# Kernel tuning notes

Measured on AMD Instinct MI355X. Metric: run time of the kernel, lower is better.

Reference implementation:

```python
import jax, jax.numpy as jnp
import numpy as np

N, E, G, Hd, Fin, L, C = 50000, 600000, 1024, 128, 74, 5, 2


def _gru(x, h, w_ih, w_hh, b_ih, b_hh):
    gi = x @ w_ih.T + b_ih
    gh = h @ w_hh.T + b_hh
    ir, iz, inn = jnp.split(gi, 3, axis=-1)
    hr, hz, hn = jnp.split(gh, 3, axis=-1)
    r = jax.nn.sigmoid(ir + hr)
    z = jax.nn.sigmoid(iz + hz)
    n = jnp.tanh(inn + r * hn)
    return (1.0 - z) * n + z * h


def _lstm_scan(xs, w_ih, w_hh, b_ih, b_hh):
    # xs: [T, B, Din]; PyTorch gate order i, f, g, o
    B = xs.shape[1]
    H = w_hh.shape[1]
    def step(carry, x):
        h, c = carry
        g = x @ w_ih.T + h @ w_hh.T + (b_ih + b_hh)
        i, f, gg, o = jnp.split(g, 4, axis=-1)
        c = jax.nn.sigmoid(f) * c + jax.nn.sigmoid(i) * jnp.tanh(gg)
        h = jax.nn.sigmoid(o) * jnp.tanh(c)
        return (h, c), h
    init = (jnp.zeros((B, H), xs.dtype), jnp.zeros((B, H), xs.dtype))
    _, ys = jax.lax.scan(step, init, xs)
    return ys


def setup_inputs():
    key = jax.random.key(0)
    ks = jax.random.split(key, 32)
    s = 0.05
    d = {}
    d['feats'] = jax.random.normal(ks[0], (N, Fin), jnp.float32)
    d['src'] = jax.random.randint(ks[1], (E,), 0, N)
    d['dst'] = jax.random.randint(ks[2], (E,), 0, N)
    d['node2graph'] = jnp.sort(jax.random.randint(ks[3], (N,), 0, G))
    d['W_in'] = jax.random.normal(ks[4], (Fin, Hd), jnp.float32) * s
    d['b_in'] = jnp.zeros((Hd,), jnp.float32)
    d['bn_gamma'] = jnp.ones((L, Hd), jnp.float32)
    d['bn_beta'] = jnp.zeros((L, Hd), jnp.float32)
    d['bn_mean'] = jax.random.normal(ks[5], (L, Hd), jnp.float32) * 0.1
    d['bn_var'] = jax.random.uniform(ks[6], (L, Hd), jnp.float32, 0.5, 1.5)
    d['gru_w_ih'] = jax.random.normal(ks[7], (3 * Hd, 2 * Hd), jnp.float32) * s
    d['gru_w_hh'] = jax.random.normal(ks[8], (3 * Hd, Hd), jnp.float32) * s
    d['gru_b_ih'] = jnp.zeros((3 * Hd,), jnp.float32)
    d['gru_b_hh'] = jnp.zeros((3 * Hd,), jnp.float32)
    d['w_aw'] = jax.random.normal(ks[9], (Hd, 1), jnp.float32) * s
    d['b_aw'] = jnp.zeros((1,), jnp.float32)
    d['lw_ih_f'] = jax.random.normal(ks[10], (4 * Hd, 2 * Hd), jnp.float32) * s
    d['lw_hh_f'] = jax.random.normal(ks[11], (4 * Hd, Hd), jnp.float32) * s
    d['lb_ih_f'] = jnp.zeros((4 * Hd,), jnp.float32)
    d['lb_hh_f'] = jnp.zeros((4 * Hd,), jnp.float32)
    d['lw_ih_b'] = jax.random.normal(ks[12], (4 * Hd, 2 * Hd), jnp.float32) * s
    d['lw_hh_b'] = jax.random.normal(ks[13], (4 * Hd, Hd), jnp.float32) * s
    d['lb_ih_b'] = jnp.zeros((4 * Hd,), jnp.float32)
    d['lb_hh_b'] = jnp.zeros((4 * Hd,), jnp.float32)
    d['W_out'] = jax.random.normal(ks[14], (2 * Hd, C), jnp.float32) * s
    d['b_out'] = jnp.zeros((C,), jnp.float32)
    return d


def reference(feats, src, dst, node2graph, W_in, b_in, bn_gamma, bn_beta, bn_mean, bn_var,
              gru_w_ih, gru_w_hh, gru_b_ih, gru_b_hh, w_aw, b_aw,
              lw_ih_f, lw_hh_f, lb_ih_f, lb_hh_f, lw_ih_b, lw_hh_b, lb_ih_b, lb_hh_b,
              W_out, b_out):
    gin_eps = 1e-5
    h = feats @ W_in + b_in  # [N, Hd]
    reps = []
    for l in range(L):
        # BatchNorm1d (eval mode, running stats)
        x = (h - bn_mean[l]) * jax.lax.rsqrt(bn_var[l] + 1e-5) * bn_gamma[l] + bn_beta[l]
        # GIN sum aggregation over edges (src -> dst)
        agg = jax.ops.segment_sum(x[src], dst, num_segments=N)  # [N, Hd]
        # GRUCell apply_func: input = concat([(1+eps)*feat, agg]), hidden = feat
        hc = _gru(jnp.concatenate([(1.0 + gin_eps) * x, agg], axis=-1), x,
                  gru_w_ih, gru_w_hh, gru_b_ih, gru_b_hh)
        hc = jax.nn.celu(hc)
        # WeightedSumAndMax readout on pre-BN feats (h)
        w = jax.nn.sigmoid(h @ w_aw + b_aw)  # [N, 1]
        ws = jax.ops.segment_sum(w * h, node2graph, num_segments=G)
        hm = jax.ops.segment_max(h, node2graph, num_segments=G)
        hm = jnp.where(jnp.isfinite(hm), hm, 0.0)
        reps.append(jnp.concatenate([ws, hm], axis=-1))  # [G, 2Hd]
        h = hc + h  # residual
    rep = jnp.stack(reps, axis=0)  # [L, G, 2Hd]
    y_f = _lstm_scan(rep, lw_ih_f, lw_hh_f, lb_ih_f, lb_hh_f)
    y_b = _lstm_scan(rep[::-1], lw_ih_b, lw_hh_b, lb_ih_b, lb_hh_b)[::-1]
    out0 = jnp.concatenate([y_f[0], y_b[0]], axis=-1)  # lstm output at t=0, [G, 2Hd]
    return out0 @ W_out + b_out  # [G, C]
```

## Files before the change

### kernel.cpp

```cpp
#include <hip/hip_runtime.h>
#include <math.h>

#define NN 50000
#define NP 50048
#define NE 600000
#define NG 1024
#define NL 5
#define NT (NP / 64)
#define GRUGRID 256

typedef __attribute__((ext_vector_type(8))) short bfrag8;
typedef __attribute__((ext_vector_type(4))) float f32x4;

__device__ __forceinline__ float fexp_(float x) { return __builtin_amdgcn_exp2f(x * 1.44269504f); }
__device__ __forceinline__ float sig_(float x)  { return __builtin_amdgcn_rcpf(1.f + fexp_(-x)); }
__device__ __forceinline__ float ftanh_(float x){ return fmaf(2.f, __builtin_amdgcn_rcpf(1.f + fexp_(-2.f * x)), -1.f); }
__device__ __forceinline__ float fexpm1_(float x){ return fexp_(x) - 1.f; }

__device__ __forceinline__ unsigned short bf16r_(float x) {
  union { float f; unsigned u; } v; v.f = x;
  unsigned u = v.u;
  return (unsigned short)((u + 0x7FFFu + ((u >> 16) & 1u)) >> 16);
}
__device__ __forceinline__ float bf16tof_(unsigned short h) {
  union { float f; unsigned u; } v; v.u = ((unsigned)h) << 16;
  return v.f;
}

__device__ __forceinline__ void gl_lds16(const unsigned short* g, unsigned short* l) {
  __builtin_amdgcn_global_load_lds(
      (const __attribute__((address_space(1))) unsigned int*)g,
      (__attribute__((address_space(3))) unsigned int*)l, 16, 0, 0);
}

__global__ __launch_bounds__(256) void k_input_proj(
    const float* __restrict__ feats, const float* __restrict__ W_in,
    const float* __restrict__ b_in, float* __restrict__ h)
{
  const int j = threadIdx.x & 127;
  const int half = threadIdx.x >> 7;
  float wcol[74];
#pragma unroll
  for (int k = 0; k < 74; ++k) wcol[k] = W_in[k * 128 + j];
  const float bj = b_in[j];
  for (int p = blockIdx.x; p < NN / 2; p += gridDim.x) {
    int node = __builtin_amdgcn_readfirstlane(p * 2 + half);
    const float* fr = feats + (size_t)node * 74;
    float acc = bj;
#pragma unroll
    for (int k = 0; k < 74; ++k) acc = fmaf(fr[k], wcol[k], acc);
    h[(size_t)node * 128 + j] = acc;
  }
}

__global__ void k_bnprep_all(const float* __restrict__ g, const float* __restrict__ b,
                             const float* __restrict__ m, const float* __restrict__ v,
                             float* __restrict__ bnp)
{
  int l = blockIdx.x;
  int j = threadIdx.x;
  float s = g[l * 128 + j] * rsqrtf(v[l * 128 + j] + 1e-5f);
  bnp[l * 256 + j] = s;
  bnp[l * 256 + 128 + j] = b[l * 128 + j] - m[l * 128 + j] * s;
}

__global__ __launch_bounds__(256) void k_wpack(
    const float* __restrict__ w_ih, const float* __restrict__ w_hh,
    const float* __restrict__ b_ih, const float* __restrict__ b_hh,
    unsigned short* __restrict__ Wp, float* __restrict__ bcat)
{
  int idx = blockIdx.x * 256 + threadIdx.x;
  int n = idx >> 8, k = idx & 255;
  float val;
  if (n < 256) {
    val = (k < 128) ? fmaf(1.00001f, w_ih[n * 256 + k], w_hh[n * 128 + k])
                    : w_ih[n * 256 + k];
  } else if (n < 384) {
    val = (k < 128) ? 1.00001f * w_ih[n * 256 + k] : w_ih[n * 256 + k];
  } else {
    int g = n - 128;
    val = (k < 128) ? w_hh[g * 128 + k] : 0.f;
  }
  Wp[(size_t)(k >> 5) * 16384 + n * 32 + (k & 31)] = bf16r_(val);
  if (k == 0) {
    float bc;
    if (n < 256) bc = b_ih[n] + b_hh[n];
    else if (n < 384) bc = b_ih[n];
    else bc = b_hh[n - 128];
    bcat[n] = bc;
  }
}

__global__ __launch_bounds__(256) void k_wpack_lstm(
    const float* __restrict__ lwih_f, const float* __restrict__ lwih_b,
    const float* __restrict__ lwhh_b,
    const float* __restrict__ lbih_f, const float* __restrict__ lbhh_f,
    const float* __restrict__ lbih_b, const float* __restrict__ lbhh_b,
    unsigned short* __restrict__ Wihf, unsigned short* __restrict__ Wihb,
    unsigned short* __restrict__ Whhb, float* __restrict__ bcf, float* __restrict__ bcb)
{
  int idx = blockIdx.x * 256 + threadIdx.x;
  if (idx < 131072) {
    int n = idx >> 8, k = idx & 255;
    Wihf[(size_t)(k >> 5) * 16384 + n * 32 + (k & 31)] = bf16r_(lwih_f[n * 256 + k]);
  } else if (idx < 262144) {
    int i2 = idx - 131072; int n = i2 >> 8, k = i2 & 255;
    Wihb[(size_t)(k >> 5) * 16384 + n * 32 + (k & 31)] = bf16r_(lwih_b[n * 256 + k]);
  } else if (idx < 327680) {
    int i2 = idx - 262144; int n = i2 >> 7, k = i2 & 127;
    Whhb[(size_t)(k >> 5) * 16384 + n * 32 + (k & 31)] = bf16r_(lwhh_b[n * 128 + k]);
  }
  if (idx < 512) {
    bcf[idx] = lbih_f[idx] + lbhh_f[idx];
    bcb[idx] = lbih_b[idx] + lbhh_b[idx];
  }
}

__global__ __launch_bounds__(256) void k_prep(
    const float* __restrict__ h, const float* __restrict__ bnp,
    const float* __restrict__ w_aw, const float* __restrict__ b_aw,
    unsigned short* __restrict__ xhi, float* __restrict__ wnode)
{
  int t = blockIdx.x * 256 + threadIdx.x;
  int row = t >> 4, c = t & 15;
  const float* hp = h + (size_t)row * 128 + c * 8;
  float4 h0 = *(const float4*)(hp);
  float4 h1 = *(const float4*)(hp + 4);
  float4 s0 = *(const float4*)(bnp + c * 8);
  float4 s1 = *(const float4*)(bnp + c * 8 + 4);
  float4 t0 = *(const float4*)(bnp + 128 + c * 8);
  float4 t1 = *(const float4*)(bnp + 128 + c * 8 + 4);
  float x[8] = { fmaf(h0.x, s0.x, t0.x), fmaf(h0.y, s0.y, t0.y),
                 fmaf(h0.z, s0.z, t0.z), fmaf(h0.w, s0.w, t0.w),
                 fmaf(h1.x, s1.x, t1.x), fmaf(h1.y, s1.y, t1.y),
                 fmaf(h1.z, s1.z, t1.z), fmaf(h1.w, s1.w, t1.w) };
  unsigned hiw[4];
#pragma unroll
  for (int i = 0; i < 4; ++i) {
    unsigned short ha = bf16r_(x[2 * i]), hb = bf16r_(x[2 * i + 1]);
    hiw[i] = (unsigned)ha | ((unsigned)hb << 16);
  }
  size_t dst = (size_t)row * 16 + (c ^ (row & 7));
  ((uint4*)xhi)[dst] = make_uint4(hiw[0], hiw[1], hiw[2], hiw[3]);
  const float4 wa0 = *(const float4*)(w_aw + c * 8);
  const float4 wa1 = *(const float4*)(w_aw + c * 8 + 4);
  float p = h0.x * wa0.x + h0.y * wa0.y + h0.z * wa0.z + h0.w * wa0.w +
            h1.x * wa1.x + h1.y * wa1.y + h1.z * wa1.z + h1.w * wa1.w;
#pragma unroll
  for (int o = 8; o > 0; o >>= 1) p += __shfl_xor(p, o);
  if (c == 0) wnode[row] = sig_(p + b_aw[0]);
}

__global__ __launch_bounds__(256) void k_hist(const int* __restrict__ dst, int* __restrict__ deg)
{
  int t = blockIdx.x * 256 + threadIdx.x;
  if (t < NE) atomicAdd(&deg[dst[t]], 1);
}

__global__ __launch_bounds__(256) void k_scan1(const int* __restrict__ deg, int* __restrict__ bsum)
{
  __shared__ int red[4];
  int i = blockIdx.x * 256 + threadIdx.x;
  int d = (i < NN) ? deg[i] : 0;
  int s = d;
#pragma unroll
  for (int o = 32; o > 0; o >>= 1) s += __shfl_xor(s, o);
  if ((threadIdx.x & 63) == 0) red[threadIdx.x >> 6] = s;
  __syncthreads();
  if (threadIdx.x == 0) bsum[blockIdx.x] = red[0] + red[1] + red[2] + red[3];
}

__global__ __launch_bounds__(256) void k_scan2(const int* __restrict__ bsum, int* __restrict__ boff,
                                               int* __restrict__ rowptr)
{
  __shared__ int part[256];
  int t = threadIdx.x;
  int v = (t < 196) ? bsum[t] : 0;
  part[t] = v;
  __syncthreads();
  for (int o = 1; o < 256; o <<= 1) {
    int u = (t >= o) ? part[t - o] : 0;
    __syncthreads();
    part[t] += u;
    __syncthreads();
  }
  if (t < 196) boff[t] = part[t] - v;
  if (t == 0) rowptr[NN] = NE;
}

__global__ __launch_bounds__(256) void k_scan3(const int* __restrict__ deg, const int* __restrict__ boff,
                                               int* __restrict__ rowptr)
{
  __shared__ int part[256];
  int t = threadIdx.x;
  int i = blockIdx.x * 256 + t;
  int d = (i < NN) ? deg[i] : 0;
  part[t] = d;
  __syncthreads();
  for (int o = 1; o < 256; o <<= 1) {
    int u = (t >= o) ? part[t - o] : 0;
    __syncthreads();
    part[t] += u;
    __syncthreads();
  }
  if (i < NN) rowptr[i] = boff[blockIdx.x] + part[t] - d;
}

__global__ __launch_bounds__(256) void k_fill(
    const int* __restrict__ src, const int* __restrict__ dst,
    int* __restrict__ pos, int* __restrict__ col)
{
  int t = blockIdx.x * 256 + threadIdx.x;
  if (t >= NE) return;
  int p = atomicAdd(&pos[dst[t]], 1);
  col[p] = src[t];
}

__global__ __launch_bounds__(256) void k_gather(
    const unsigned short* __restrict__ xhi, const int* __restrict__ rowptr,
    const int* __restrict__ col, unsigned short* __restrict__ agghi)
{
  int n = blockIdx.x * 4 + (threadIdx.x >> 6);
  int lane = threadIdx.x & 63;
  int c = lane >> 2, q = lane & 3;
  int lo = rowptr[n], hi = rowptr[n + 1];
  const unsigned* xp = (const unsigned*)xhi;
  float a0 = 0.f, a1 = 0.f, a2 = 0.f, a3 = 0.f;
  float b0 = 0.f, b1 = 0.f, b2 = 0.f, b3 = 0.f;
  int e = lo;
  for (; e + 3 < hi; e += 4) {
    int r0 = col[e], r1 = col[e + 1], r2 = col[e + 2], r3 = col[e + 3];
    unsigned u0 = xp[(size_t)r0 * 64 + ((c ^ (r0 & 7)) << 2) + q];
    unsigned u1 = xp[(size_t)r1 * 64 + ((c ^ (r1 & 7)) << 2) + q];
    unsigned u2 = xp[(size_t)r2 * 64 + ((c ^ (r2 & 7)) << 2) + q];
    unsigned u3 = xp[(size_t)r3 * 64 + ((c ^ (r3 & 7)) << 2) + q];
    a0 += bf16tof_((unsigned short)(u0 & 0xFFFF)); b0 += bf16tof_((unsigned short)(u0 >> 16));
    a1 += bf16tof_((unsigned short)(u1 & 0xFFFF)); b1 += bf16tof_((unsigned short)(u1 >> 16));
    a2 += bf16tof_((unsigned short)(u2 & 0xFFFF)); b2 += bf16tof_((unsigned short)(u2 >> 16));
    a3 += bf16tof_((unsigned short)(u3 & 0xFFFF)); b3 += bf16tof_((unsigned short)(u3 >> 16));
  }
  for (; e < hi; ++e) {
    int r0 = col[e];
    unsigned u0 = xp[(size_t)r0 * 64 + ((c ^ (r0 & 7)) << 2) + q];
    a0 += bf16tof_((unsigned short)(u0 & 0xFFFF));
    b0 += bf16tof_((unsigned short)(u0 >> 16));
  }
  float s0 = (a0 + a1) + (a2 + a3), s1 = (b0 + b1) + (b2 + b3);
  unsigned short h0 = bf16r_(s0), h1 = bf16r_(s1);
  size_t w = (size_t)n * 64 + ((c ^ (n & 7)) << 2) + q;
  ((unsigned*)agghi)[w] = (unsigned)h0 | ((unsigned)h1 << 16);
}

__device__ __forceinline__ int lbound_(const int* __restrict__ a, int n, int key)
{
  int lo = 0, hi = n;
  while (lo < hi) { int mid = (lo + hi) >> 1; if (a[mid] < key) lo = mid + 1; else hi = mid; }
  return lo;
}

__global__ __launch_bounds__(256) void k_readout(
    const float* __restrict__ h, const float* __restrict__ wnode,
    const int* __restrict__ n2g, unsigned short* __restrict__ xplh,
    unsigned short* __restrict__ xpll, int layer)
{
  __shared__ float WS[128], HM[128];
  int g = blockIdx.x;
  int tid = threadIdx.x;
  int j = tid & 127, ty = tid >> 7;
  int lo = lbound_(n2g, NN, g);
  int hi = lbound_(n2g, NN, g + 1);
  float ws0 = 0.f, hm0 = -INFINITY, ws1 = 0.f, hm1 = -INFINITY;
  int n = lo + ty;
  for (; n + 2 < hi; n += 4) {
    float hv0 = h[(size_t)n * 128 + j];
    float hv1 = h[(size_t)(n + 2) * 128 + j];
    ws0 = fmaf(wnode[n], hv0, ws0);     hm0 = fmaxf(hm0, hv0);
    ws1 = fmaf(wnode[n + 2], hv1, ws1); hm1 = fmaxf(hm1, hv1);
  }
  if (n < hi) {
    float hv0 = h[(size_t)n * 128 + j];
    ws0 = fmaf(wnode[n], hv0, ws0); hm0 = fmaxf(hm0, hv0);
  }
  float ws = ws0 + ws1, hm = fmaxf(hm0, hm1);
  if (ty == 1) { WS[j] = ws; HM[j] = hm; }
  __syncthreads();
  if (ty == 0) {
    ws += WS[j];
    hm = fmaxf(hm, HM[j]);
    if (hi == lo) hm = 0.f;
    int r = layer * NG + g;
    {
      unsigned short hi16 = bf16r_(ws);
      unsigned short lo16 = bf16r_(ws - bf16tof_(hi16));
      size_t si = (size_t)r * 256 + (((j >> 3) ^ (r & 7)) << 3) + (j & 7);
      xplh[si] = hi16; xpll[si] = lo16;
    }
    {
      int ch = 128 + j;
      unsigned short hi16 = bf16r_(hm);
      unsigned short lo16 = bf16r_(hm - bf16tof_(hi16));
      size_t si = (size_t)r * 256 + (((ch >> 3) ^ (r & 7)) << 3) + (ch & 7);
      xplh[si] = hi16; xpll[si] = lo16;
    }
  }
}

__global__ __launch_bounds__(512, 2) void k_gru_mfma(
    float* __restrict__ h,
    const unsigned short* __restrict__ xhi, const unsigned short* __restrict__ agghi,
    const unsigned short* __restrict__ Wp, const float* __restrict__ bcat,
    const float* __restrict__ bnp)
{
  __shared__ alignas(16) unsigned short A[2][16384];
  const int tid = threadIdx.x;
  const int lane = tid & 63;
  const int wv = tid >> 6;
  const int mfr = lane & 15;
  const int kq = lane >> 4;
  const int j = wv * 16 + mfr;

  bfrag8 wreg[8][4];
#pragma unroll
  for (int kb = 0; kb < 8; ++kb) {
    int ng = (kb < 4) ? 4 : 3;
#pragma unroll
    for (int g = 0; g < 4; ++g) {
      if (g < ng) {
        int n = g * 128 + j;
        wreg[kb][g] = *(const bfrag8*)(Wp + (size_t)kb * 16384 + n * 32 + kq * 8);
      }
    }
  }

  auto stage = [&](int buf, int tile) {
    size_t goff = (size_t)tile * 64 * 128;
    const unsigned short* srcs[2] = { xhi + goff, agghi + goff };
#pragma unroll
    for (int p = 0; p < 2; ++p) {
#pragma unroll
      for (int it = 0; it < 2; ++it) {
        int off = it * 4096 + wv * 512;
        gl_lds16(srcs[p] + off + lane * 8, &A[buf][p * 8192 + off]);
      }
    }
  };

  const float sc = bnp[j], sh = bnp[128 + j];
  const float br = bcat[j], bz = bcat[128 + j], bi = bcat[256 + j], bh = bcat[384 + j];

  int tile = blockIdx.x;
  stage(0, tile);
  __syncthreads();
  int cur = 0;

  while (true) {
    int nxt = tile + GRUGRID;
    int m0 = tile * 64;

    float hvr[4][4];
#pragma unroll
    for (int m = 0; m < 4; ++m)
#pragma unroll
      for (int reg = 0; reg < 4; ++reg)
        hvr[m][reg] = h[(size_t)(m0 + m * 16 + kq * 4 + reg) * 128 + j];

    if (nxt < NT) stage(cur ^ 1, nxt);

    f32x4 acc[4][4];
#pragma unroll
    for (int m = 0; m < 4; ++m)
#pragma unroll
      for (int g = 0; g < 4; ++g) acc[m][g] = (f32x4){0.f, 0.f, 0.f, 0.f};

    const char* Ab = (const char*)&A[cur][0];
#pragma unroll
    for (int kb = 0; kb < 8; ++kb) {
      int kp = kb & 3;
      int hoff = (kb < 4) ? 0 : 16384;
      int ng = (kb < 4) ? 4 : 3;
      bfrag8 ah[4];
#pragma unroll
      for (int m = 0; m < 4; ++m) {
        int row = m * 16 + mfr;
        int cs = (((kp * 4 + kq) ^ (row & 7)) << 4);
        ah[m] = *(const bfrag8*)(Ab + hoff + row * 256 + cs);
      }
#pragma unroll
      for (int m = 0; m < 4; ++m)
#pragma unroll
        for (int g = 0; g < 4; ++g) {
          if (g < ng)
            acc[m][g] = __builtin_amdgcn_mfma_f32_16x16x32_bf16(ah[m], wreg[kb][g], acc[m][g], 0, 0, 0);
        }
    }

    float hnew[4][4];
#pragma unroll
    for (int m = 0; m < 4; ++m) {
#pragma unroll
      for (int reg = 0; reg < 4; ++reg) {
        float hvv = hvr[m][reg];
        float x = fmaf(hvv, sc, sh);
        float r = sig_(acc[m][0][reg] + br);
        float z = sig_(acc[m][1][reg] + bz);
        float n2 = ftanh_(fmaf(r, acc[m][3][reg] + bh, acc[m][2][reg] + bi));
        float o = (1.f - z) * n2 + z * x;
        float hc = (o > 0.f) ? o : fexpm1_(o);
        hnew[m][reg] = hvv + hc;
      }
    }

    __syncthreads();

    float* Hst = (float*)&A[cur][0];
#pragma unroll
    for (int m = 0; m < 4; ++m)
#pragma unroll
      for (int reg = 0; reg < 4; ++reg) {
        int nl = m * 16 + kq * 4 + reg;
        Hst[nl * 128 + (j ^ ((nl & 7) << 2))] = hnew[m][reg];
      }

    __syncthreads();

    {
      float* dst = h + (size_t)m0 * 128;
#pragma unroll
      for (int p = 0; p < 4; ++p) {
        int b = p * 2048 + tid * 4;
        int row = b >> 7;
        int off = b & 127;
        float4 v = *(const float4*)&Hst[row * 128 + (off ^ ((row & 7) << 2))];
        *(float4*)&dst[b] = v;
      }
    }

    if (nxt >= NT) break;
    __syncthreads();
    cur ^= 1;
    tile = nxt;
  }
}

__global__ __launch_bounds__(512) void k_xgates(
    const unsigned short* __restrict__ xplh, const unsigned short* __restrict__ xpll,
    const unsigned short* __restrict__ Wihb, const unsigned short* __restrict__ Wihf,
    const float* __restrict__ bcb, const float* __restrict__ bcf,
    float* __restrict__ gxb, float* __restrict__ gxf)
{
  __shared__ alignas(16) unsigned short Ah[16384], Al[16384];
  int bid = blockIdx.x;
  const unsigned short* Wp; const float* bc; float* gx; int r0;
  if (bid < 80) { Wp = Wihb; bc = bcb; gx = gxb; r0 = bid * 64; }
  else          { Wp = Wihf; bc = bcf; gx = gxf; r0 = (bid - 80) * 64; }
  const int tid = threadIdx.x;
  const int lane = tid & 63;
  const int wv = tid >> 6;
  const int mfr = lane & 15;
  const int kq = lane >> 4;
  const int j = wv * 16 + mfr;

#pragma unroll
  for (int q = 0; q < 4; ++q) {
    int off = (q * 512 + wv * 64) * 8;
    gl_lds16(xplh + (size_t)r0 * 256 + off + lane * 8, &Ah[off]);
    gl_lds16(xpll + (size_t)r0 * 256 + off + lane * 8, &Al[off]);
  }

  bfrag8 wr[8][4];
#pragma unroll
  for (int kb = 0; kb < 8; ++kb)
#pragma unroll
    for (int g = 0; g < 4; ++g) {
      int n = g * 128 + j;
      wr[kb][g] = *(const bfrag8*)(Wp + (size_t)kb * 16384 + n * 32 + kq * 8);
    }

  __syncthreads();

  f32x4 acc[4][4];
#pragma unroll
  for (int m = 0; m < 4; ++m)
#pragma unroll
    for (int g = 0; g < 4; ++g) acc[m][g] = (f32x4){0.f, 0.f, 0.f, 0.f};

  const char* Ab = (const char*)Ah;
  const char* Al8 = (const char*)Al;
#pragma unroll
  for (int kb = 0; kb < 8; ++kb) {
    bfrag8 ah[4], al[4];
#pragma unroll
    for (int m = 0; m < 4; ++m) {
      int rr = m * 16 + mfr;
      int cs = ((((kb * 4 + kq)) ^ (rr & 7)) << 4);
      ah[m] = *(const bfrag8*)(Ab + rr * 512 + cs);
      al[m] = *(const bfrag8*)(Al8 + rr * 512 + cs);
    }
#pragma unroll
    for (int m = 0; m < 4; ++m)
#pragma unroll
      for (int g = 0; g < 4; ++g) {
        acc[m][g] = __builtin_amdgcn_mfma_f32_16x16x32_bf16(ah[m], wr[kb][g], acc[m][g], 0, 0, 0);
        acc[m][g] = __builtin_amdgcn_mfma_f32_16x16x32_bf16(al[m], wr[kb][g], acc[m][g], 0, 0, 0);
      }
  }

#pragma unroll
  for (int g = 0; g < 4; ++g) {
    float b = bc[g * 128 + j];
#pragma unroll
    for (int m = 0; m < 4; ++m)
#pragma unroll
      for (int reg = 0; reg < 4; ++reg) {
        int rr = m * 16 + kq * 4 + reg;
        gx[((size_t)(r0 + rr)) * 512 + g * 128 + j] = acc[m][g][reg] + b;
      }
  }
}

__global__ __launch_bounds__(256) void k_lstm0(const float* __restrict__ gxf, float* __restrict__ yf)
{
  int i = blockIdx.x * 256 + threadIdx.x;
  int row = i >> 7, j = i & 127;
  const float* gp = gxf + (size_t)row * 512;
  float cn = sig_(gp[j]) * ftanh_(gp[256 + j]);
  yf[i] = sig_(gp[384 + j]) * ftanh_(cn);
}

__global__ __launch_bounds__(512) void k_lstm_rec(
    const float* __restrict__ gxb, const unsigned short* __restrict__ Whh,
    float* __restrict__ yb)
{
  __shared__ alignas(16) unsigned short Hh[4096], Hl[4096];
  const int tid = threadIdx.x;
  const int lane = tid & 63;
  const int wv = tid >> 6;
  const int mfr = lane & 15;
  const int kq = lane >> 4;
  const int r0 = blockIdx.x * 32;
  const int j = wv * 16 + mfr;

  bfrag8 whh[4][4];
#pragma unroll
  for (int kb = 0; kb < 4; ++kb)
#pragma unroll
    for (int g = 0; g < 4; ++g) {
      int n = g * 128 + j;
      whh[kb][g] = *(const bfrag8*)(Whh + (size_t)kb * 16384 + n * 32 + kq * 8);
    }

  float cc[2][4];
#pragma unroll
  for (int m = 0; m < 2; ++m)
#pragma unroll
    for (int reg = 0; reg < 4; ++reg) {
      int rr = m * 16 + kq * 4 + reg;
      const float* gp = gxb + ((size_t)(4 * NG) + r0 + rr) * 512;
      float cn = sig_(gp[j]) * ftanh_(gp[256 + j]);
      cc[m][reg] = cn;
      float hh = sig_(gp[384 + j]) * ftanh_(cn);
      unsigned short hb16 = bf16r_(hh);
      unsigned short lb16 = bf16r_(hh - bf16tof_(hb16));
      int si = rr * 128 + (((j >> 3) ^ (rr & 7)) << 3) + (j & 7);
      Hh[si] = hb16; Hl[si] = lb16;
    }
  __syncthreads();

  for (int t = 3; t >= 0; --t) {
    f32x4 acc[2][4];
#pragma unroll
    for (int m = 0; m < 2; ++m)
#pragma unroll
      for (int g = 0; g < 4; ++g) acc[m][g] = (f32x4){0.f, 0.f, 0.f, 0.f};
    const char* Bh = (const char*)Hh;
    const char* Bl = (const char*)Hl;
#pragma unroll
    for (int kb = 0; kb < 4; ++kb) {
      bfrag8 ah[2], al[2];
#pragma unroll
      for (int m = 0; m < 2; ++m) {
        int rr = m * 16 + mfr;
        int cs = (((kb * 4 + kq) ^ (rr & 7)) << 4);
        ah[m] = *(const bfrag8*)(Bh + rr * 256 + cs);
        al[m] = *(const bfrag8*)(Bl + rr * 256 + cs);
      }
#pragma unroll
      for (int m = 0; m < 2; ++m)
#pragma unroll
        for (int g = 0; g < 4; ++g) {
          acc[m][g] = __builtin_amdgcn_mfma_f32_16x16x32_bf16(ah[m], whh[kb][g], acc[m][g], 0, 0, 0);
          acc[m][g] = __builtin_amdgcn_mfma_f32_16x16x32_bf16(al[m], whh[kb][g], acc[m][g], 0, 0, 0);
        }
    }
    __syncthreads();
#pragma unroll
    for (int m = 0; m < 2; ++m)
#pragma unroll
      for (int reg = 0; reg < 4; ++reg) {
        int rr = m * 16 + kq * 4 + reg;
        const float* gp = gxb + ((size_t)(t * NG) + r0 + rr) * 512;
        float g0 = acc[m][0][reg] + gp[j];
        float g1 = acc[m][1][reg] + gp[128 + j];
        float g2 = acc[m][2][reg] + gp[256 + j];
        float g3 = acc[m][3][reg] + gp[384 + j];
        float cn = fmaf(sig_(g1), cc[m][reg], sig_(g0) * ftanh_(g2));
        cc[m][reg] = cn;
        float hh = sig_(g3) * ftanh_(cn);
        if (t > 0) {
          unsigned short hb16 = bf16r_(hh);
          unsigned short lb16 = bf16r_(hh - bf16tof_(hb16));
          int si = rr * 128 + (((j >> 3) ^ (rr & 7)) << 3) + (j & 7);
          Hh[si] = hb16; Hl[si] = lb16;
        } else {
          yb[(size_t)(r0 + rr) * 128 + j] = hh;
        }
      }
    if (t > 0) __syncthreads();
  }
}

__global__ __launch_bounds__(256) void k_final(
    const float* __restrict__ yf, const float* __restrict__ yb,
    const float* __restrict__ W_out, const float* __restrict__ b_out,
    float* __restrict__ out)
{
  int tid = threadIdx.x;
  int g = blockIdx.x * 4 + (tid >> 6);
  int lane = tid & 63;
  float a0 = 0.f, a1 = 0.f;
  for (int k = lane; k < 128; k += 64) {
    float v = yf[g * 128 + k];
    a0 = fmaf(v, W_out[k * 2 + 0], a0);
    a1 = fmaf(v, W_out[k * 2 + 1], a1);
    float u = yb[g * 128 + k];
    a0 = fmaf(u, W_out[(128 + k) * 2 + 0], a0);
    a1 = fmaf(u, W_out[(128 + k) * 2 + 1], a1);
  }
#pragma unroll
  for (int o = 32; o > 0; o >>= 1) { a0 += __shfl_xor(a0, o); a1 += __shfl_xor(a1, o); }
  if (lane == 0) {
    out[g * 2 + 0] = a0 + b_out[0];
    out[g * 2 + 1] = a1 + b_out[1];
  }
}

extern "C" void kernel_launch(void* const* d_in, const int* in_sizes, int n_in,
                              void* d_out, int out_size, void* d_ws, size_t ws_size,
                              hipStream_t stream)
{
  (void)in_sizes; (void)n_in; (void)out_size; (void)ws_size;
  const float* feats   = (const float*)d_in[0];
  const int*   src     = (const int*)d_in[1];
  const int*   dst     = (const int*)d_in[2];
  const int*   n2g     = (const int*)d_in[3];
  const float* W_in    = (const float*)d_in[4];
  const float* b_in    = (const float*)d_in[5];
  const float* bng     = (const float*)d_in[6];
  const float* bnb     = (const float*)d_in[7];
  const float* bnm     = (const float*)d_in[8];
  const float* bnv     = (const float*)d_in[9];
  const float* gw_ih   = (const float*)d_in[10];
  const float* gw_hh   = (const float*)d_in[11];
  const float* gb_ih   = (const float*)d_in[12];
  const float* gb_hh   = (const float*)d_in[13];
  const float* w_aw    = (const float*)d_in[14];
  const float* b_aw    = (const float*)d_in[15];
  const float* lwih_f  = (const float*)d_in[16];
  const float* lwhh_f  = (const float*)d_in[17];
  const float* lbih_f  = (const float*)d_in[18];
  const float* lbhh_f  = (const float*)d_in[19];
  const float* lwih_b  = (const float*)d_in[20];
  const float* lwhh_b  = (const float*)d_in[21];
  const float* lbih_b  = (const float*)d_in[22];
  const float* lbhh_b  = (const float*)d_in[23];
  const float* W_out   = (const float*)d_in[24];
  const float* b_out   = (const float*)d_in[25];
  float* out = (float*)d_out;
  (void)lwhh_f;

  float* ws = (float*)d_ws;
  size_t off = 0;
  auto alloc = [&](size_t n) { float* p = ws + off; off += (n + 63) & ~(size_t)63; return p; };
  float* h      = alloc((size_t)NP * 128);
  unsigned short* xhi   = (unsigned short*)alloc((size_t)NP * 64);
  unsigned short* agghi = (unsigned short*)alloc((size_t)NP * 64);
  unsigned short* Wp    = (unsigned short*)alloc(65536);
  float* bcat   = alloc(512);
  float* wnode  = alloc(NN);
  float* bnp    = alloc(NL * 256);
  unsigned short* xplh = (unsigned short*)alloc((size_t)NL * NG * 128);
  unsigned short* xpll = (unsigned short*)alloc((size_t)NL * NG * 128);
  unsigned short* Wihf = (unsigned short*)alloc(65536);
  unsigned short* Wihb = (unsigned short*)alloc(65536);
  unsigned short* Whhb = (unsigned short*)alloc(32768);
  float* bcf    = alloc(512);
  float* bcb    = alloc(512);
  float* gxb    = alloc((size_t)NL * NG * 512);
  float* gxf    = alloc((size_t)NG * 512);
  float* yf     = alloc((size_t)NG * 128);
  float* yb     = alloc((size_t)NG * 128);
  int* deg    = (int*)alloc(NN);
  int* rowptr = (int*)alloc(NN + 1);
  int* pos    = (int*)alloc(NN);
  int* colidx = (int*)alloc(NE);
  int* bsum   = (int*)alloc(256);
  int* boff   = (int*)alloc(256);

  hipMemsetAsync(deg, 0, (size_t)NN * sizeof(int), stream);
  k_hist<<<(NE + 255) / 256, 256, 0, stream>>>(dst, deg);
  k_scan1<<<196, 256, 0, stream>>>(deg, bsum);
  k_scan2<<<1, 256, 0, stream>>>(bsum, boff, rowptr);
  k_scan3<<<196, 256, 0, stream>>>(deg, boff, rowptr);
  hipMemcpyAsync(pos, rowptr, (size_t)NN * sizeof(int), hipMemcpyDeviceToDevice, stream);
  k_fill<<<(NE + 255) / 256, 256, 0, stream>>>(src, dst, pos, colidx);
  k_wpack<<<512, 256, 0, stream>>>(gw_ih, gw_hh, gb_ih, gb_hh, Wp, bcat);
  k_wpack_lstm<<<1280, 256, 0, stream>>>(lwih_f, lwih_b, lwhh_b, lbih_f, lbhh_f, lbih_b, lbhh_b,
                                         Wihf, Wihb, Whhb, bcf, bcb);
  k_bnprep_all<<<NL, 128, 0, stream>>>(bng, bnb, bnm, bnv, bnp);

  k_input_proj<<<1024, 256, 0, stream>>>(feats, W_in, b_in, h);

  for (int l = 0; l < NL; ++l) {
    const float* bnpl = bnp + l * 256;
    k_prep<<<3125, 256, 0, stream>>>(h, bnpl, w_aw, b_aw, xhi, wnode);
    k_gather<<<NN / 4, 256, 0, stream>>>(xhi, rowptr, colidx, agghi);
    k_readout<<<NG, 256, 0, stream>>>(h, wnode, n2g, xplh, xpll, l);
    k_gru_mfma<<<GRUGRID, 512, 0, stream>>>(h, xhi, agghi, Wp, bcat, bnpl);
  }

  k_xgates<<<96, 512, 0, stream>>>(xplh, xpll, Wihb, Wihf, bcb, bcf, gxb, gxf);
  k_lstm0<<<512, 256, 0, stream>>>(gxf, yf);
  k_lstm_rec<<<32, 512, 0, stream>>>(gxb, Whhb, yb);

  k_final<<<NG / 4, 256, 0, stream>>>(yf, yb, W_out, b_out, out);
}
```

Measured before the change: 566.0 us.

## Fuse per-layer BN/bf16 prep into the input projection and GRU epilogue

```diff
diff --git a/kernel.cpp b/kernel.cpp
--- a/kernel.cpp
+++ b/kernel.cpp
@@ -35,21 +35,38 @@
 
 __global__ __launch_bounds__(256) void k_input_proj(
     const float* __restrict__ feats, const float* __restrict__ W_in,
-    const float* __restrict__ b_in, float* __restrict__ h)
-{
-  const int j = threadIdx.x & 127;
-  const int half = threadIdx.x >> 7;
-  float wcol[74];
-#pragma unroll
-  for (int k = 0; k < 74; ++k) wcol[k] = W_in[k * 128 + j];
-  const float bj = b_in[j];
-  for (int p = blockIdx.x; p < NN / 2; p += gridDim.x) {
-    int node = __builtin_amdgcn_readfirstlane(p * 2 + half);
+    const float* __restrict__ b_in, const float* __restrict__ bnp0,
+    const float* __restrict__ w_aw, const float* __restrict__ b_aw,
+    float* __restrict__ h, unsigned short* __restrict__ xhi, float* __restrict__ wnode)
+{
+  const int lane = threadIdx.x & 63;
+  const int wv = threadIdx.x >> 6;
+  const int j0 = lane, j1 = lane + 64;
+  float wc0[74], wc1[74];
+#pragma unroll
+  for (int k = 0; k < 74; ++k) { wc0[k] = W_in[k * 128 + j0]; wc1[k] = W_in[k * 128 + j1]; }
+  const float bj0 = b_in[j0], bj1 = b_in[j1];
+  const float sc0 = bnp0[j0], sh0 = bnp0[128 + j0];
+  const float sc1 = bnp0[j1], sh1 = bnp0[128 + j1];
+  const float wa0 = w_aw[j0], wa1 = w_aw[j1];
+  const float baw = b_aw[0];
+  for (int p = blockIdx.x; p < NN / 4; p += gridDim.x) {
+    int node = __builtin_amdgcn_readfirstlane(p * 4 + wv);
     const float* fr = feats + (size_t)node * 74;
-    float acc = bj;
-#pragma unroll
-    for (int k = 0; k < 74; ++k) acc = fmaf(fr[k], wcol[k], acc);
-    h[(size_t)node * 128 + j] = acc;
+    float a0 = bj0, a1 = bj1;
+#pragma unroll
+    for (int k = 0; k < 74; ++k) { float f = fr[k]; a0 = fmaf(f, wc0[k], a0); a1 = fmaf(f, wc1[k], a1); }
+    h[(size_t)node * 128 + j0] = a0;
+    h[(size_t)node * 128 + j1] = a1;
+    float x0 = fmaf(a0, sc0, sh0), x1 = fmaf(a1, sc1, sh1);
+    char* xrowp = (char*)(xhi + (size_t)node * 128);
+    int s = node & 7;
+    *(unsigned short*)(xrowp + ((((j0 >> 3) ^ s)) << 4) + (j0 & 7) * 2) = bf16r_(x0);
+    *(unsigned short*)(xrowp + ((((j1 >> 3) ^ s)) << 4) + (j1 & 7) * 2) = bf16r_(x1);
+    float pw = a0 * wa0 + a1 * wa1;
+#pragma unroll
+    for (int o = 32; o > 0; o >>= 1) pw += __shfl_xor(pw, o);
+    if (lane == 0) wnode[node] = sig_(pw + baw);
   }
 }
 
@@ -116,41 +133,6 @@
   }
 }
 
-__global__ __launch_bounds__(256) void k_prep(
-    const float* __restrict__ h, const float* __restrict__ bnp,
-    const float* __restrict__ w_aw, const float* __restrict__ b_aw,
-    unsigned short* __restrict__ xhi, float* __restrict__ wnode)
-{
-  int t = blockIdx.x * 256 + threadIdx.x;
-  int row = t >> 4, c = t & 15;
-  const float* hp = h + (size_t)row * 128 + c * 8;
-  float4 h0 = *(const float4*)(hp);
-  float4 h1 = *(const float4*)(hp + 4);
-  float4 s0 = *(const float4*)(bnp + c * 8);
-  float4 s1 = *(const float4*)(bnp + c * 8 + 4);
-  float4 t0 = *(const float4*)(bnp + 128 + c * 8);
-  float4 t1 = *(const float4*)(bnp + 128 + c * 8 + 4);
-  float x[8] = { fmaf(h0.x, s0.x, t0.x), fmaf(h0.y, s0.y, t0.y),
-                 fmaf(h0.z, s0.z, t0.z), fmaf(h0.w, s0.w, t0.w),
-                 fmaf(h1.x, s1.x, t1.x), fmaf(h1.y, s1.y, t1.y),
-                 fmaf(h1.z, s1.z, t1.z), fmaf(h1.w, s1.w, t1.w) };
-  unsigned hiw[4];
-#pragma unroll
-  for (int i = 0; i < 4; ++i) {
-    unsigned short ha = bf16r_(x[2 * i]), hb = bf16r_(x[2 * i + 1]);
-    hiw[i] = (unsigned)ha | ((unsigned)hb << 16);
-  }
-  size_t dst = (size_t)row * 16 + (c ^ (row & 7));
-  ((uint4*)xhi)[dst] = make_uint4(hiw[0], hiw[1], hiw[2], hiw[3]);
-  const float4 wa0 = *(const float4*)(w_aw + c * 8);
-  const float4 wa1 = *(const float4*)(w_aw + c * 8 + 4);
-  float p = h0.x * wa0.x + h0.y * wa0.y + h0.z * wa0.z + h0.w * wa0.w +
-            h1.x * wa1.x + h1.y * wa1.y + h1.z * wa1.z + h1.w * wa1.w;
-#pragma unroll
-  for (int o = 8; o > 0; o >>= 1) p += __shfl_xor(p, o);
-  if (c == 0) wnode[row] = sig_(p + b_aw[0]);
-}
-
 __global__ __launch_bounds__(256) void k_hist(const int* __restrict__ dst, int* __restrict__ deg)
 {
   int t = blockIdx.x * 256 + threadIdx.x;
@@ -189,7 +171,7 @@
 }
 
 __global__ __launch_bounds__(256) void k_scan3(const int* __restrict__ deg, const int* __restrict__ boff,
-                                               int* __restrict__ rowptr)
+                                               int* __restrict__ rowptr, int* __restrict__ pos)
 {
   __shared__ int part[256];
   int t = threadIdx.x;
@@ -203,7 +185,11 @@
     part[t] += u;
     __syncthreads();
   }
-  if (i < NN) rowptr[i] = boff[blockIdx.x] + part[t] - d;
+  if (i < NN) {
+    int v = boff[blockIdx.x] + part[t] - d;
+    rowptr[i] = v;
+    pos[i] = v;
+  }
 }
 
 __global__ __launch_bounds__(256) void k_fill(
@@ -307,9 +293,11 @@
 
 __global__ __launch_bounds__(512, 2) void k_gru_mfma(
     float* __restrict__ h,
-    const unsigned short* __restrict__ xhi, const unsigned short* __restrict__ agghi,
+    unsigned short* __restrict__ xhi, const unsigned short* __restrict__ agghi,
     const unsigned short* __restrict__ Wp, const float* __restrict__ bcat,
-    const float* __restrict__ bnp)
+    const float* __restrict__ bnp, const float* __restrict__ bnpn,
+    const float* __restrict__ w_aw, const float* __restrict__ b_aw,
+    float* __restrict__ wnode)
 {
   __shared__ alignas(16) unsigned short A[2][16384];
   const int tid = threadIdx.x;
@@ -347,6 +335,11 @@
 
   const float sc = bnp[j], sh = bnp[128 + j];
   const float br = bcat[j], bz = bcat[128 + j], bi = bcat[256 + j], bh = bcat[384 + j];
+  const int offc = (tid * 4) & 127;
+  const float4 scn = *(const float4*)&bnpn[offc];
+  const float4 shn = *(const float4*)&bnpn[128 + offc];
+  const float4 wa  = *(const float4*)&w_aw[offc];
+  const float baw = b_aw[0];
 
   int tile = blockIdx.x;
   stage(0, tile);
@@ -429,9 +422,23 @@
       for (int p = 0; p < 4; ++p) {
         int b = p * 2048 + tid * 4;
         int row = b >> 7;
-        int off = b & 127;
-        float4 v = *(const float4*)&Hst[row * 128 + (off ^ ((row & 7) << 2))];
+        float4 v = *(const float4*)&Hst[row * 128 + (offc ^ ((row & 7) << 2))];
         *(float4*)&dst[b] = v;
+        float x0 = fmaf(v.x, scn.x, shn.x), x1 = fmaf(v.y, scn.y, shn.y);
+        float x2 = fmaf(v.z, scn.z, shn.z), x3 = fmaf(v.w, scn.w, shn.w);
+        uint2 xv;
+        xv.x = (unsigned)bf16r_(x0) | ((unsigned)bf16r_(x1) << 16);
+        xv.y = (unsigned)bf16r_(x2) | ((unsigned)bf16r_(x3) << 16);
+        char* xrowp = (char*)(xhi + (size_t)(m0 + row) * 128);
+        int c = offc >> 3;
+        *(uint2*)(xrowp + (((c ^ (row & 7))) << 4) + (offc & 7) * 2) = xv;
+        float pw = v.x * wa.x + v.y * wa.y + v.z * wa.z + v.w * wa.w;
+#pragma unroll
+        for (int o = 16; o > 0; o >>= 1) pw += __shfl_xor(pw, o);
+        if ((lane & 31) == 0) {
+          int node = m0 + row;
+          if (node < NN) wnode[node] = sig_(pw + baw);
+        }
       }
     }
 
@@ -710,22 +717,21 @@
   k_hist<<<(NE + 255) / 256, 256, 0, stream>>>(dst, deg);
   k_scan1<<<196, 256, 0, stream>>>(deg, bsum);
   k_scan2<<<1, 256, 0, stream>>>(bsum, boff, rowptr);
-  k_scan3<<<196, 256, 0, stream>>>(deg, boff, rowptr);
-  hipMemcpyAsync(pos, rowptr, (size_t)NN * sizeof(int), hipMemcpyDeviceToDevice, stream);
+  k_scan3<<<196, 256, 0, stream>>>(deg, boff, rowptr, pos);
   k_fill<<<(NE + 255) / 256, 256, 0, stream>>>(src, dst, pos, colidx);
   k_wpack<<<512, 256, 0, stream>>>(gw_ih, gw_hh, gb_ih, gb_hh, Wp, bcat);
   k_wpack_lstm<<<1280, 256, 0, stream>>>(lwih_f, lwih_b, lwhh_b, lbih_f, lbhh_f, lbih_b, lbhh_b,
                                          Wihf, Wihb, Whhb, bcf, bcb);
   k_bnprep_all<<<NL, 128, 0, stream>>>(bng, bnb, bnm, bnv, bnp);
 
-  k_input_proj<<<1024, 256, 0, stream>>>(feats, W_in, b_in, h);
+  k_input_proj<<<1024, 256, 0, stream>>>(feats, W_in, b_in, bnp, w_aw, b_aw, h, xhi, wnode);
 
   for (int l = 0; l < NL; ++l) {
     const float* bnpl = bnp + l * 256;
-    k_prep<<<3125, 256, 0, stream>>>(h, bnpl, w_aw, b_aw, xhi, wnode);
+    const float* bnpn = bnp + ((l < NL - 1) ? (l + 1) : l) * 256;
     k_gather<<<NN / 4, 256, 0, stream>>>(xhi, rowptr, colidx, agghi);
     k_readout<<<NG, 256, 0, stream>>>(h, wnode, n2g, xplh, xpll, l);
-    k_gru_mfma<<<GRUGRID, 512, 0, stream>>>(h, xhi, agghi, Wp, bcat, bnpl);
+    k_gru_mfma<<<GRUGRID, 512, 0, stream>>>(h, xhi, agghi, Wp, bcat, bnpl, bnpn, w_aw, b_aw, wnode);
   }
 
   k_xgates<<<96, 512, 0, stream>>>(xplh, xpll, Wihb, Wihf, bcb, bcf, gxb, gxf);
```

Result: slower. 658.7 us (+16.4%).

## Fuse per-layer prep into GRU epilogue and merge gather with readout

Applied to the files above, without the earlier changes.

```diff
diff --git a/kernel.cpp b/kernel.cpp
--- a/kernel.cpp
+++ b/kernel.cpp
@@ -189,7 +189,7 @@
 }
 
 __global__ __launch_bounds__(256) void k_scan3(const int* __restrict__ deg, const int* __restrict__ boff,
-                                               int* __restrict__ rowptr)
+                                               int* __restrict__ rowptr, int* __restrict__ pos)
 {
   __shared__ int part[256];
   int t = threadIdx.x;
@@ -203,7 +203,11 @@
     part[t] += u;
     __syncthreads();
   }
-  if (i < NN) rowptr[i] = boff[blockIdx.x] + part[t] - d;
+  if (i < NN) {
+    int v = boff[blockIdx.x] + part[t] - d;
+    rowptr[i] = v;
+    pos[i] = v;
+  }
 }
 
 __global__ __launch_bounds__(256) void k_fill(
@@ -216,41 +220,6 @@
   col[p] = src[t];
 }
 
-__global__ __launch_bounds__(256) void k_gather(
-    const unsigned short* __restrict__ xhi, const int* __restrict__ rowptr,
-    const int* __restrict__ col, unsigned short* __restrict__ agghi)
-{
-  int n = blockIdx.x * 4 + (threadIdx.x >> 6);
-  int lane = threadIdx.x & 63;
-  int c = lane >> 2, q = lane & 3;
-  int lo = rowptr[n], hi = rowptr[n + 1];
-  const unsigned* xp = (const unsigned*)xhi;
-  float a0 = 0.f, a1 = 0.f, a2 = 0.f, a3 = 0.f;
-  float b0 = 0.f, b1 = 0.f, b2 = 0.f, b3 = 0.f;
-  int e = lo;
-  for (; e + 3 < hi; e += 4) {
-    int r0 = col[e], r1 = col[e + 1], r2 = col[e + 2], r3 = col[e + 3];
-    unsigned u0 = xp[(size_t)r0 * 64 + ((c ^ (r0 & 7)) << 2) + q];
-    unsigned u1 = xp[(size_t)r1 * 64 + ((c ^ (r1 & 7)) << 2) + q];
-    unsigned u2 = xp[(size_t)r2 * 64 + ((c ^ (r2 & 7)) << 2) + q];
-    unsigned u3 = xp[(size_t)r3 * 64 + ((c ^ (r3 & 7)) << 2) + q];
-    a0 += bf16tof_((unsigned short)(u0 & 0xFFFF)); b0 += bf16tof_((unsigned short)(u0 >> 16));
-    a1 += bf16tof_((unsigned short)(u1 & 0xFFFF)); b1 += bf16tof_((unsigned short)(u1 >> 16));
-    a2 += bf16tof_((unsigned short)(u2 & 0xFFFF)); b2 += bf16tof_((unsigned short)(u2 >> 16));
-    a3 += bf16tof_((unsigned short)(u3 & 0xFFFF)); b3 += bf16tof_((unsigned short)(u3 >> 16));
-  }
-  for (; e < hi; ++e) {
-    int r0 = col[e];
-    unsigned u0 = xp[(size_t)r0 * 64 + ((c ^ (r0 & 7)) << 2) + q];
-    a0 += bf16tof_((unsigned short)(u0 & 0xFFFF));
-    b0 += bf16tof_((unsigned short)(u0 >> 16));
-  }
-  float s0 = (a0 + a1) + (a2 + a3), s1 = (b0 + b1) + (b2 + b3);
-  unsigned short h0 = bf16r_(s0), h1 = bf16r_(s1);
-  size_t w = (size_t)n * 64 + ((c ^ (n & 7)) << 2) + q;
-  ((unsigned*)agghi)[w] = (unsigned)h0 | ((unsigned)h1 << 16);
-}
-
 __device__ __forceinline__ int lbound_(const int* __restrict__ a, int n, int key)
 {
   int lo = 0, hi = n;
@@ -258,60 +227,98 @@
   return lo;
 }
 
-__global__ __launch_bounds__(256) void k_readout(
+__global__ __launch_bounds__(256) void k_gr(
+    const unsigned short* __restrict__ xhi, const int* __restrict__ rowptr,
+    const int* __restrict__ col, unsigned short* __restrict__ agghi,
     const float* __restrict__ h, const float* __restrict__ wnode,
     const int* __restrict__ n2g, unsigned short* __restrict__ xplh,
     unsigned short* __restrict__ xpll, int layer)
 {
   __shared__ float WS[128], HM[128];
-  int g = blockIdx.x;
-  int tid = threadIdx.x;
-  int j = tid & 127, ty = tid >> 7;
-  int lo = lbound_(n2g, NN, g);
-  int hi = lbound_(n2g, NN, g + 1);
-  float ws0 = 0.f, hm0 = -INFINITY, ws1 = 0.f, hm1 = -INFINITY;
-  int n = lo + ty;
-  for (; n + 2 < hi; n += 4) {
-    float hv0 = h[(size_t)n * 128 + j];
-    float hv1 = h[(size_t)(n + 2) * 128 + j];
-    ws0 = fmaf(wnode[n], hv0, ws0);     hm0 = fmaxf(hm0, hv0);
-    ws1 = fmaf(wnode[n + 2], hv1, ws1); hm1 = fmaxf(hm1, hv1);
-  }
-  if (n < hi) {
-    float hv0 = h[(size_t)n * 128 + j];
-    ws0 = fmaf(wnode[n], hv0, ws0); hm0 = fmaxf(hm0, hv0);
-  }
-  float ws = ws0 + ws1, hm = fmaxf(hm0, hm1);
-  if (ty == 1) { WS[j] = ws; HM[j] = hm; }
-  __syncthreads();
-  if (ty == 0) {
-    ws += WS[j];
-    hm = fmaxf(hm, HM[j]);
-    if (hi == lo) hm = 0.f;
-    int r = layer * NG + g;
-    {
-      unsigned short hi16 = bf16r_(ws);
-      unsigned short lo16 = bf16r_(ws - bf16tof_(hi16));
-      size_t si = (size_t)r * 256 + (((j >> 3) ^ (r & 7)) << 3) + (j & 7);
-      xplh[si] = hi16; xpll[si] = lo16;
-    }
-    {
-      int ch = 128 + j;
-      unsigned short hi16 = bf16r_(hm);
-      unsigned short lo16 = bf16r_(hm - bf16tof_(hi16));
-      size_t si = (size_t)r * 256 + (((ch >> 3) ^ (r & 7)) << 3) + (ch & 7);
-      xplh[si] = hi16; xpll[si] = lo16;
+  int bid = blockIdx.x;
+  if (bid < NN / 4) {
+    int n = bid * 4 + (threadIdx.x >> 6);
+    int lane = threadIdx.x & 63;
+    int c = lane >> 2, q = lane & 3;
+    int lo = rowptr[n], hi = rowptr[n + 1];
+    const unsigned* xp = (const unsigned*)xhi;
+    float a0 = 0.f, a1 = 0.f, a2 = 0.f, a3 = 0.f;
+    float b0 = 0.f, b1 = 0.f, b2 = 0.f, b3 = 0.f;
+    int e = lo;
+    for (; e + 3 < hi; e += 4) {
+      int r0 = col[e], r1 = col[e + 1], r2 = col[e + 2], r3 = col[e + 3];
+      unsigned u0 = xp[(size_t)r0 * 64 + ((c ^ (r0 & 7)) << 2) + q];
+      unsigned u1 = xp[(size_t)r1 * 64 + ((c ^ (r1 & 7)) << 2) + q];
+      unsigned u2 = xp[(size_t)r2 * 64 + ((c ^ (r2 & 7)) << 2) + q];
+      unsigned u3 = xp[(size_t)r3 * 64 + ((c ^ (r3 & 7)) << 2) + q];
+      a0 += bf16tof_((unsigned short)(u0 & 0xFFFF)); b0 += bf16tof_((unsigned short)(u0 >> 16));
+      a1 += bf16tof_((unsigned short)(u1 & 0xFFFF)); b1 += bf16tof_((unsigned short)(u1 >> 16));
+      a2 += bf16tof_((unsigned short)(u2 & 0xFFFF)); b2 += bf16tof_((unsigned short)(u2 >> 16));
+      a3 += bf16tof_((unsigned short)(u3 & 0xFFFF)); b3 += bf16tof_((unsigned short)(u3 >> 16));
+    }
+    for (; e < hi; ++e) {
+      int r0 = col[e];
+      unsigned u0 = xp[(size_t)r0 * 64 + ((c ^ (r0 & 7)) << 2) + q];
+      a0 += bf16tof_((unsigned short)(u0 & 0xFFFF));
+      b0 += bf16tof_((unsigned short)(u0 >> 16));
+    }
+    float s0 = (a0 + a1) + (a2 + a3), s1 = (b0 + b1) + (b2 + b3);
+    unsigned short h0 = bf16r_(s0), h1 = bf16r_(s1);
+    size_t w = (size_t)n * 64 + ((c ^ (n & 7)) << 2) + q;
+    ((unsigned*)agghi)[w] = (unsigned)h0 | ((unsigned)h1 << 16);
+  } else {
+    int g = bid - NN / 4;
+    int tid = threadIdx.x;
+    int j = tid & 127, ty = tid >> 7;
+    int lo = lbound_(n2g, NN, g);
+    int hi = lbound_(n2g, NN, g + 1);
+    float ws0 = 0.f, hm0 = -INFINITY, ws1 = 0.f, hm1 = -INFINITY;
+    int n = lo + ty;
+    for (; n + 2 < hi; n += 4) {
+      float hv0 = h[(size_t)n * 128 + j];
+      float hv1 = h[(size_t)(n + 2) * 128 + j];
+      ws0 = fmaf(wnode[n], hv0, ws0);     hm0 = fmaxf(hm0, hv0);
+      ws1 = fmaf(wnode[n + 2], hv1, ws1); hm1 = fmaxf(hm1, hv1);
+    }
+    if (n < hi) {
+      float hv0 = h[(size_t)n * 128 + j];
+      ws0 = fmaf(wnode[n], hv0, ws0); hm0 = fmaxf(hm0, hv0);
+    }
+    float ws = ws0 + ws1, hm = fmaxf(hm0, hm1);
+    if (ty == 1) { WS[j] = ws; HM[j] = hm; }
+    __syncthreads();
+    if (ty == 0) {
+      ws += WS[j];
+      hm = fmaxf(hm, HM[j]);
+      if (hi == lo) hm = 0.f;
+      int r = layer * NG + g;
+      {
+        unsigned short hi16 = bf16r_(ws);
+        unsigned short lo16 = bf16r_(ws - bf16tof_(hi16));
+        size_t si = (size_t)r * 256 + (((j >> 3) ^ (r & 7)) << 3) + (j & 7);
+        xplh[si] = hi16; xpll[si] = lo16;
+      }
+      {
+        int ch = 128 + j;
+        unsigned short hi16 = bf16r_(hm);
+        unsigned short lo16 = bf16r_(hm - bf16tof_(hi16));
+        size_t si = (size_t)r * 256 + (((ch >> 3) ^ (r & 7)) << 3) + (ch & 7);
+        xplh[si] = hi16; xpll[si] = lo16;
+      }
     }
   }
 }
 
 __global__ __launch_bounds__(512, 2) void k_gru_mfma(
     float* __restrict__ h,
-    const unsigned short* __restrict__ xhi, const unsigned short* __restrict__ agghi,
+    unsigned short* __restrict__ xhi, const unsigned short* __restrict__ agghi,
     const unsigned short* __restrict__ Wp, const float* __restrict__ bcat,
-    const float* __restrict__ bnp)
+    const float* __restrict__ bnp, const float* __restrict__ bnpn,
+    const float* __restrict__ w_aw, const float* __restrict__ b_aw,
+    float* __restrict__ wnode, int emit)
 {
   __shared__ alignas(16) unsigned short A[2][16384];
+  __shared__ alignas(16) unsigned short X[8192];
   const int tid = threadIdx.x;
   const int lane = tid & 63;
   const int wv = tid >> 6;
@@ -347,6 +354,11 @@
 
   const float sc = bnp[j], sh = bnp[128 + j];
   const float br = bcat[j], bz = bcat[128 + j], bi = bcat[256 + j], bh = bcat[384 + j];
+  const int offc = (tid * 4) & 127;
+  const float4 scn = *(const float4*)&bnpn[offc];
+  const float4 shn = *(const float4*)&bnpn[128 + offc];
+  const float4 wa  = *(const float4*)&w_aw[offc];
+  const float baw = b_aw[0];
 
   int tile = blockIdx.x;
   stage(0, tile);
@@ -429,10 +441,32 @@
       for (int p = 0; p < 4; ++p) {
         int b = p * 2048 + tid * 4;
         int row = b >> 7;
-        int off = b & 127;
-        float4 v = *(const float4*)&Hst[row * 128 + (off ^ ((row & 7) << 2))];
+        float4 v = *(const float4*)&Hst[row * 128 + (offc ^ ((row & 7) << 2))];
         *(float4*)&dst[b] = v;
-      }
+        if (emit) {
+          float x0 = fmaf(v.x, scn.x, shn.x), x1 = fmaf(v.y, scn.y, shn.y);
+          float x2 = fmaf(v.z, scn.z, shn.z), x3 = fmaf(v.w, scn.w, shn.w);
+          uint2 xv;
+          xv.x = (unsigned)bf16r_(x0) | ((unsigned)bf16r_(x1) << 16);
+          xv.y = (unsigned)bf16r_(x2) | ((unsigned)bf16r_(x3) << 16);
+          *(uint2*)((char*)X + row * 256 + ((((offc >> 3) ^ (row & 7))) << 4) + (offc & 7) * 2) = xv;
+          float pw = v.x * wa.x + v.y * wa.y + v.z * wa.z + v.w * wa.w;
+#pragma unroll
+          for (int o = 16; o > 0; o >>= 1) pw += __shfl_xor(pw, o);
+          if ((lane & 31) == 0) {
+            int node = m0 + row;
+            if (node < NN) wnode[node] = sig_(pw + baw);
+          }
+        }
+      }
+    }
+
+    if (emit) {
+      __syncthreads();
+      uint4* Xg = (uint4*)(xhi + (size_t)m0 * 128);
+      const uint4* Xl = (const uint4*)X;
+      Xg[tid * 2] = Xl[tid * 2];
+      Xg[tid * 2 + 1] = Xl[tid * 2 + 1];
     }
 
     if (nxt >= NT) break;
@@ -686,7 +720,7 @@
   unsigned short* agghi = (unsigned short*)alloc((size_t)NP * 64);
   unsigned short* Wp    = (unsigned short*)alloc(65536);
   float* bcat   = alloc(512);
-  float* wnode  = alloc(NN);
+  float* wnode  = alloc(NP);
   float* bnp    = alloc(NL * 256);
   unsigned short* xplh = (unsigned short*)alloc((size_t)NL * NG * 128);
   unsigned short* xpll = (unsigned short*)alloc((size_t)NL * NG * 128);
@@ -710,8 +744,7 @@
   k_hist<<<(NE + 255) / 256, 256, 0, stream>>>(dst, deg);
   k_scan1<<<196, 256, 0, stream>>>(deg, bsum);
   k_scan2<<<1, 256, 0, stream>>>(bsum, boff, rowptr);
-  k_scan3<<<196, 256, 0, stream>>>(deg, boff, rowptr);
-  hipMemcpyAsync(pos, rowptr, (size_t)NN * sizeof(int), hipMemcpyDeviceToDevice, stream);
+  k_scan3<<<196, 256, 0, stream>>>(deg, boff, rowptr, pos);
   k_fill<<<(NE + 255) / 256, 256, 0, stream>>>(src, dst, pos, colidx);
   k_wpack<<<512, 256, 0, stream>>>(gw_ih, gw_hh, gb_ih, gb_hh, Wp, bcat);
   k_wpack_lstm<<<1280, 256, 0, stream>>>(lwih_f, lwih_b, lwhh_b, lbih_f, lbhh_f, lbih_b, lbhh_b,
@@ -719,13 +752,14 @@
   k_bnprep_all<<<NL, 128, 0, stream>>>(bng, bnb, bnm, bnv, bnp);
 
   k_input_proj<<<1024, 256, 0, stream>>>(feats, W_in, b_in, h);
+  k_prep<<<3125, 256, 0, stream>>>(h, bnp, w_aw, b_aw, xhi, wnode);
 
   for (int l = 0; l < NL; ++l) {
     const float* bnpl = bnp + l * 256;
-    k_prep<<<3125, 256, 0, stream>>>(h, bnpl, w_aw, b_aw, xhi, wnode);
-    k_gather<<<NN / 4, 256, 0, stream>>>(xhi, rowptr, colidx, agghi);
-    k_readout<<<NG, 256, 0, stream>>>(h, wnode, n2g, xplh, xpll, l);
-    k_gru_mfma<<<GRUGRID, 512, 0, stream>>>(h, xhi, agghi, Wp, bcat, bnpl);
+    const float* bnpn = bnp + ((l < NL - 1) ? (l + 1) : l) * 256;
+    k_gr<<<NN / 4 + NG, 256, 0, stream>>>(xhi, rowptr, colidx, agghi, h, wnode, n2g, xplh, xpll, l);
+    k_gru_mfma<<<GRUGRID, 512, 0, stream>>>(h, xhi, agghi, Wp, bcat, bnpl, bnpn, w_aw, b_aw,
+                                            wnode, (l < NL - 1) ? 1 : 0);
   }
 
   k_xgates<<<96, 512, 0, stream>>>(xplh, xpll, Wihb, Wihf, bcb, bcf, gxb, gxf);
```

Result: slower. 602.3 us (+6.4%).
